# Kernel tuning notes

Hardware: AMD Instinct MI355X
Metric: run time of the kernel (lower is better)

Reference implementation:

```python
import jax, jax.numpy as jnp
from jax import lax
import numpy as np

GRID, IMG, BLOCK = 60, 960, 16
BN_EPS = 1e-5


def _conv(x, w, b):
    return lax.conv_general_dilated(x, w, (1, 1), 'SAME', dimension_numbers=('NCHW', 'OIHW', 'NCHW')) + b[None, :, None, None]


def _bn(x, g, b):
    # inference BatchNorm with running_mean=0, running_var=1
    s = g * np.float32(1.0 / np.sqrt(1.0 + BN_EPS))
    return x * s[None, :, None, None] + b[None, :, None, None]


def _mlp(x, w1, b1, w2, b2):
    return jax.nn.relu(x @ w1.T + b1) @ w2.T + b2


def _lstm_layer(x, wih, whh, b):
    # x: [B,T,D]; torch gate order i,f,g,o; zero initial state
    B = x.shape[0]
    H = whh.shape[1]
    pre = jnp.swapaxes(x, 0, 1) @ wih.T + b  # [T,B,4H]

    def step(carry, p):
        h, c = carry
        z = p + h @ whh.T
        i, f, g, o = jnp.split(z, 4, axis=-1)
        c = jax.nn.sigmoid(f) * c + jax.nn.sigmoid(i) * jnp.tanh(g)
        h = jax.nn.sigmoid(o) * jnp.tanh(c)
        return (h, c), h

    z0 = jnp.zeros((B, H), x.dtype)
    (h, c), ys = lax.scan(step, (z0, z0), pre)
    return jnp.swapaxes(ys, 0, 1), h, c


def _forward(motion_vectors, boxes, track_ids, conv1_w, conv1_b, bn1_g, bn1_b, conv2_w, conv2_b, bn2_g, bn2_b, conv3_w, conv3_b, bn3_g, bn3_b, agg_w1, agg_b1, agg_w2, agg_b2, bx_w1, bx_b1, bx_w2, bx_b2, id_table, proj_w, proj_b, empty_slot, l0_wih, l0_whh, l0_b, l1_wih, l1_whh, l1_b, hb_w1, hb_b1, hb_w2, hb_b2, hc_w1, hc_b1, hc_w2, hc_b2, ht_w1, ht_b1, ht_w2, ht_b2):
    B = motion_vectors.shape[0]
    # ---- grid encoder (Conv-BN-ReLU x3) ----
    x = jax.nn.relu(_bn(_conv(motion_vectors, conv1_w, conv1_b), bn1_g, bn1_b))
    x = jax.nn.relu(_bn(_conv(x, conv2_w, conv2_b), bn2_g, bn2_b))
    gf = jax.nn.relu(_bn(_conv(x, conv3_w, conv3_b), bn3_g, bn3_b))  # [B,64,60,60]
    global_feat = gf.mean((-2, -1))  # AdaptiveAvgPool2d(1) -> [B,64]

    # ---- per-box motion statistics (vectorized masked reductions) ----
    bg = jnp.clip(boxes * (IMG / BLOCK), 0.0, GRID - 1e-6)  # grid coords
    ix1 = jnp.floor(bg[..., 0]); iy1 = jnp.floor(bg[..., 1])
    ix2 = jnp.maximum(ix1 + 1.0, jnp.ceil(bg[..., 2]))
    iy2 = jnp.maximum(iy1 + 1.0, jnp.ceil(bg[..., 3]))
    g = jnp.arange(GRID, dtype=bg.dtype)
    mx_ = (g >= ix1[..., None]) & (g < ix2[..., None])  # [B,N,60]
    my_ = (g >= iy1[..., None]) & (g < iy2[..., None])
    mask = my_[..., :, None] & mx_[..., None, :]  # [B,N,60,60]
    m = mask.astype(bg.dtype)
    cnt = m.sum((-2, -1))[..., None]  # [B,N,1], >= 1 by construction
    mv = motion_vectors  # [B,2,60,60]
    s1 = jnp.einsum('bnyx,bcyx->bnc', m, mv)
    s2 = jnp.einsum('bnyx,bcyx->bnc', m, mv * mv)
    mean = s1 / cnt
    var = (s2 - cnt * mean * mean) / jnp.maximum(cnt - 1.0, 1.0)  # unbiased, like torch .std()
    var_safe = jnp.where(cnt > 1.0, jnp.maximum(var, 1e-12), 1.0)
    std = jnp.where(cnt > 1.0, jnp.sqrt(var_safe), 0.0)
    BIG = jnp.asarray(1e9, bg.dtype)
    mn = jnp.min(jnp.where(mask[:, :, None], mv[:, None], BIG), axis=(-2, -1))   # [B,N,2]
    mx = jnp.max(jnp.where(mask[:, :, None], mv[:, None], -BIG), axis=(-2, -1))  # [B,N,2]
    stats = jnp.stack([mean[..., 0], mean[..., 1], std[..., 0], std[..., 1], mn[..., 0], mx[..., 0], mn[..., 1], mx[..., 1]], -1)  # [B,N,8]
    motion_emb = _mlp(stats, agg_w1, agg_b1, agg_w2, agg_b2)  # [B,N,64]

    # ---- slot initialization ----
    box_emb = _mlp(boxes, bx_w1, bx_b1, bx_w2, bx_b2)  # [B,N,64]
    id_emb = id_table[jnp.clip(track_ids, 0, 999)]  # [B,N,32]
    obj = jnp.concatenate([box_emb, id_emb, motion_emb], -1)  # [B,N,160]
    slots = obj @ proj_w.T + proj_b  # [B,300,128]; N == max_slots so no empty slots used

    # ---- 2-layer LSTM over the 300 slots (batch_first, eval -> no dropout) ----
    Ns = slots.shape[1]
    gexp = jnp.broadcast_to(global_feat[:, None, :], (B, Ns, global_feat.shape[-1]))
    lstm_in = jnp.concatenate([slots, gexp], -1)  # [B,300,192]
    y, h0, c0 = _lstm_layer(lstm_in, l0_wih, l0_whh, l0_b)
    y, h1, c1 = _lstm_layer(y, l1_wih, l1_whh, l1_b)  # [B,300,128]

    # ---- RT-DETR style heads ----
    pred_boxes = jax.nn.sigmoid(_mlp(y, hb_w1, hb_b1, hb_w2, hb_b2))  # [B,300,4]
    cls_logits = _mlp(y, hc_w1, hc_b1, hc_w2, hc_b2)  # [B,300,2]
    tid_logits = _mlp(y, ht_w1, ht_b1, ht_w2, ht_b2)  # [B,300,1000]
    h = jnp.stack([h0, h1])
    c = jnp.stack([c0, c1])
    return pred_boxes, cls_logits, tid_logits, h, c


def setup_inputs() -> dict:
    B, N = 32, 300
    key = jax.random.key(0)
    ks = iter(jax.random.split(key, 60))

    def w(*s):
        return jax.random.normal(next(ks), s, jnp.float32) * 0.05

    mv = jax.random.normal(next(ks), (B, 2, GRID, GRID), jnp.float32)
    bb = jax.random.uniform(next(ks), (B, N, 4), jnp.float32)
    boxes = jnp.concatenate([jnp.minimum(bb[..., :2], bb[..., 2:]), jnp.maximum(bb[..., :2], bb[..., 2:])], -1)
    track_ids = jax.random.randint(next(ks), (B, N), 0, 1000)
    return dict(
        motion_vectors=mv, boxes=boxes, track_ids=track_ids,
        conv1_w=w(32, 2, 3, 3), conv1_b=w(32), bn1_g=1.0 + w(32), bn1_b=w(32),
        conv2_w=w(64, 32, 3, 3), conv2_b=w(64), bn2_g=1.0 + w(64), bn2_b=w(64),
        conv3_w=w(64, 64, 3, 3), conv3_b=w(64), bn3_g=1.0 + w(64), bn3_b=w(64),
        agg_w1=w(32, 8), agg_b1=w(32), agg_w2=w(64, 32), agg_b2=w(64),
        bx_w1=w(32, 4), bx_b1=w(32), bx_w2=w(64, 32), bx_b2=w(64),
        id_table=w(1000, 32).at[0].set(0.0),
        proj_w=w(128, 160), proj_b=w(128), empty_slot=w(128),
        l0_wih=w(512, 192), l0_whh=w(512, 128), l0_b=w(512),
        l1_wih=w(512, 128), l1_whh=w(512, 128), l1_b=w(512),
        hb_w1=w(256, 128), hb_b1=w(256), hb_w2=w(4, 256), hb_b2=w(4),
        hc_w1=w(256, 128), hc_b1=w(256), hc_w2=w(2, 256), hc_b2=w(2),
        ht_w1=w(256, 128), ht_b1=w(256), ht_w2=w(1000, 256), ht_b2=w(1000))


def reference(motion_vectors, boxes, track_ids, conv1_w, conv1_b, bn1_g, bn1_b, conv2_w, conv2_b, bn2_g, bn2_b, conv3_w, conv3_b, bn3_g, bn3_b, agg_w1, agg_b1, agg_w2, agg_b2, bx_w1, bx_b1, bx_w2, bx_b2, id_table, proj_w, proj_b, empty_slot, l0_wih, l0_whh, l0_b, l1_wih, l1_whh, l1_b, hb_w1, hb_b1, hb_w2, hb_b2, hc_w1, hc_b1, hc_w2, hc_b2, ht_w1, ht_b1, ht_w2, ht_b2):
    return _forward(motion_vectors, boxes, track_ids, conv1_w, conv1_b, bn1_g, bn1_b, conv2_w, conv2_b, bn2_g, bn2_b, conv3_w, conv3_b, bn3_g, bn3_b, agg_w1, agg_b1, agg_w2, agg_b2, bx_w1, bx_b1, bx_w2, bx_b2, id_table, proj_w, proj_b, empty_slot, l0_wih, l0_whh, l0_b, l1_wih, l1_whh, l1_b, hb_w1, hb_b1, hb_w2, hb_b2, hc_w1, hc_b1, hc_w2, hc_b2, ht_w1, ht_b1, ht_w2, ht_b2)
```

## Files before the change

### kernel.cpp

```cpp
#include <hip/hip_runtime.h>
#include <hip/hip_bf16.h>
#include <math.h>

typedef unsigned short ushort_t;
typedef __attribute__((ext_vector_type(8))) short bf16x8;
typedef __attribute__((ext_vector_type(4))) float f32x4;

#define LOG2E 1.4426950408889634f

__device__ __forceinline__ float sigf(float x) {
  x = fminf(fmaxf(x, -30.f), 30.f);
  return 1.f / (1.f + __expf(-x));
}
__device__ __forceinline__ ushort_t f2bf(float x) {
  unsigned int b = __float_as_uint(x);
  unsigned int lsb = (b >> 16) & 1u;
  b += 0x7fffu + lsb;
  return (ushort_t)(b >> 16);
}
__device__ __forceinline__ float bf2f(ushort_t u) {
  return __uint_as_float(((unsigned int)u) << 16);
}
__device__ __forceinline__ float gsc(int g3) {
  return (g3 == 2) ? (2.f * LOG2E) : LOG2E;
}

#define NPIX 3600
__device__ __forceinline__ int gperm(int rho) {
  return ((rho & 3) << 7) + (rho >> 2);
}

__global__ __launch_bounds__(256) void front_kernel(
    const float* __restrict__ mv, const float* __restrict__ boxes,
    const int* __restrict__ ids, const float* __restrict__ agg_w1,
    const float* __restrict__ agg_b1, const float* __restrict__ agg_w2,
    const float* __restrict__ agg_b2, const float* __restrict__ bx_w1,
    const float* __restrict__ bx_b1, const float* __restrict__ bx_w2,
    const float* __restrict__ bx_b2, const float* __restrict__ id_table,
    ushort_t* __restrict__ obj_out, const float* __restrict__ conv2_w,
    const float* __restrict__ conv3_w, const float* __restrict__ wih0,
    const float* __restrict__ projW, const float* __restrict__ projb,
    const float* __restrict__ l0_b, const float* __restrict__ hbw1,
    const float* __restrict__ hcw1, const float* __restrict__ htw1,
    const float* __restrict__ htw2, const float* __restrict__ hbb1,
    const float* __restrict__ hcb1, const float* __restrict__ htb1,
    ushort_t* __restrict__ wc2, ushort_t* __restrict__ wc3,
    ushort_t* __restrict__ wAp, float* __restrict__ l0bp,
    ushort_t* __restrict__ whid, ushort_t* __restrict__ wt2,
    float* __restrict__ bhid) {
  if (blockIdx.x < 1989) {
    int i = blockIdx.x * 256 + threadIdx.x;
    if (i < 18432) {
      int oc = i / 288, r = i % 288, kt = r / 32, ic = r % 32;
      wc2[i] = f2bf(conv2_w[((oc * 32 + ic) * 3 + kt / 3) * 3 + kt % 3]);
      return;
    }
    i -= 18432;
    if (i < 36864) {
      int oc = i / 576, r = i % 576, c = r / 288, r2 = r % 288;
      int kt = r2 / 32, icl = r2 % 32, ic = c * 32 + icl;
      wc3[i] = f2bf(conv3_w[((oc * 64 + ic) * 3 + kt / 3) * 3 + kt % 3]);
      return;
    }
    i -= 36864;
    if (i < 98304) {
      int n = i / 192, k = i % 192;
      int src = gperm(n);
      float a = 0.f;
      if (k < 160) {
        const float* wr = wih0 + src * 192;
        for (int j = 0; j < 128; ++j) a = fmaf(wr[j], projW[j * 160 + k], a);
      }
      wAp[i] = f2bf(a * gsc(n & 3));
      return;
    }
    i -= 98304;
    if (i < 512) {
      int src = gperm(i);
      float a = l0_b[src];
      const float* wr = wih0 + src * 192;
      for (int j = 0; j < 128; ++j) a = fmaf(wr[j], projb[j], a);
      l0bp[i] = a * gsc(i & 3);
      return;
    }
    i -= 512;
    if (i < 98304) {
      int row = i >> 7, c = i & 127;
      float v = (row < 256)   ? hbw1[row * 128 + c]
                : (row < 512) ? hcw1[(row - 256) * 128 + c]
                              : htw1[(row - 512) * 128 + c];
      whid[i] = f2bf(v);
      return;
    }
    i -= 98304;
    if (i < 256000) {
      wt2[i] = f2bf(htw2[i]);
      return;
    }
    i -= 256000;
    if (i < 768)
      bhid[i] = (i < 256) ? hbb1[i] : (i < 512) ? hcb1[i - 256] : htb1[i - 512];
    return;
  }
  int bx = blockIdx.x - 1989;
  __shared__ float obj[2][160];
  __shared__ float hm[2][32];
  __shared__ float hbx[2][32];
  __shared__ float stats[2][8];
  __shared__ float boxf[2][4];
  __shared__ float red[2][2][8];
  int h = threadIdx.x >> 7;
  int t = threadIdx.x & 127;
  int blk = bx * 2 + h;
  int b = blk / 300;
  float bx0 = boxes[blk * 4 + 0], by0 = boxes[blk * 4 + 1];
  float bx1 = boxes[blk * 4 + 2], by1 = boxes[blk * 4 + 3];
  const float HI = (float)(60.0 - 1e-6);
  float gx1 = fminf(fmaxf(bx0 * 60.f, 0.f), HI);
  float gy1 = fminf(fmaxf(by0 * 60.f, 0.f), HI);
  float gx2 = fminf(fmaxf(bx1 * 60.f, 0.f), HI);
  float gy2 = fminf(fmaxf(by1 * 60.f, 0.f), HI);
  float fx1 = floorf(gx1), fy1 = floorf(gy1);
  float fx2 = fmaxf(fx1 + 1.f, ceilf(gx2));
  float fy2 = fmaxf(fy1 + 1.f, ceilf(gy2));
  int ix1 = (int)fx1, iy1 = (int)fy1, ix2 = (int)fx2, iy2 = (int)fy2;
  int w = ix2 - ix1, hgt = iy2 - iy1;
  int area = w * hgt;
  float s0 = 0.f, s1 = 0.f, q0 = 0.f, q1 = 0.f;
  float mn0 = 1e9f, mn1 = 1e9f, mx0 = -1e9f, mx1 = -1e9f;
  const float* mv0 = mv + b * 2 * NPIX;
  const float* mv1 = mv0 + NPIX;
  for (int i = t; i < area; i += 128) {
    int r = i / w, cc = i - r * w;
    int yy = iy1 + r, xx = ix1 + cc;
    float v0 = mv0[yy * 60 + xx];
    float v1 = mv1[yy * 60 + xx];
    s0 += v0; q0 += v0 * v0; mn0 = fminf(mn0, v0); mx0 = fmaxf(mx0, v0);
    s1 += v1; q1 += v1 * v1; mn1 = fminf(mn1, v1); mx1 = fmaxf(mx1, v1);
  }
#pragma unroll
  for (int off = 32; off; off >>= 1) {
    s0 += __shfl_down(s0, off); s1 += __shfl_down(s1, off);
    q0 += __shfl_down(q0, off); q1 += __shfl_down(q1, off);
    mn0 = fminf(mn0, __shfl_down(mn0, off));
    mn1 = fminf(mn1, __shfl_down(mn1, off));
    mx0 = fmaxf(mx0, __shfl_down(mx0, off));
    mx1 = fmaxf(mx1, __shfl_down(mx1, off));
  }
  if ((t & 63) == 0) {
    int wv = t >> 6;
    red[h][wv][0] = s0; red[h][wv][1] = s1;
    red[h][wv][2] = q0; red[h][wv][3] = q1;
    red[h][wv][4] = mn0; red[h][wv][5] = mn1;
    red[h][wv][6] = mx0; red[h][wv][7] = mx1;
  }
  __syncthreads();
  if (t == 0) {
    float S0 = red[h][0][0] + red[h][1][0], S1 = red[h][0][1] + red[h][1][1];
    float Q0 = red[h][0][2] + red[h][1][2], Q1 = red[h][0][3] + red[h][1][3];
    float MN0 = fminf(red[h][0][4], red[h][1][4]);
    float MN1 = fminf(red[h][0][5], red[h][1][5]);
    float MX0 = fmaxf(red[h][0][6], red[h][1][6]);
    float MX1 = fmaxf(red[h][0][7], red[h][1][7]);
    float cnt = (float)area;
    float mean0 = S0 / cnt, mean1 = S1 / cnt;
    float var0 = (Q0 - cnt * mean0 * mean0) / fmaxf(cnt - 1.f, 1.f);
    float var1 = (Q1 - cnt * mean1 * mean1) / fmaxf(cnt - 1.f, 1.f);
    float sd0 = (cnt > 1.f) ? sqrtf(fmaxf(var0, 1e-12f)) : 0.f;
    float sd1 = (cnt > 1.f) ? sqrtf(fmaxf(var1, 1e-12f)) : 0.f;
    stats[h][0] = mean0; stats[h][1] = mean1; stats[h][2] = sd0;
    stats[h][3] = sd1; stats[h][4] = MN0; stats[h][5] = MX0;
    stats[h][6] = MN1; stats[h][7] = MX1;
    boxf[h][0] = bx0; boxf[h][1] = by0; boxf[h][2] = bx1; boxf[h][3] = by1;
  }
  __syncthreads();
  if (t < 32) {
    float a = agg_b1[t];
#pragma unroll
    for (int k = 0; k < 8; ++k) a = fmaf(stats[h][k], agg_w1[t * 8 + k], a);
    hm[h][t] = fmaxf(a, 0.f);
  } else if (t < 64) {
    int j = t - 32;
    float a = bx_b1[j];
#pragma unroll
    for (int k = 0; k < 4; ++k) a = fmaf(boxf[h][k], bx_w1[j * 4 + k], a);
    hbx[h][j] = fmaxf(a, 0.f);
  }
  __syncthreads();
  if (t < 64) {
    float a = bx_b2[t];
#pragma unroll
    for (int k = 0; k < 32; ++k) a = fmaf(hbx[h][k], bx_w2[t * 32 + k], a);
    obj[h][t] = a;
  } else {
    int j = t - 64;
    float a = agg_b2[j];
#pragma unroll
    for (int k = 0; k < 32; ++k) a = fmaf(hm[h][k], agg_w2[j * 32 + k], a);
    obj[h][96 + j] = a;
  }
  if (t < 32) {
    int id = ids[blk];
    id = min(max(id, 0), 999);
    obj[h][64 + t] = id_table[id * 32 + t];
  }
  __syncthreads();
  obj_out[(size_t)blk * 192 + t] = f2bf(obj[h][t]);
  if (t < 32) {
    obj_out[(size_t)blk * 192 + 128 + t] = f2bf(obj[h][128 + t]);
    obj_out[(size_t)blk * 192 + 160 + t] = 0;
  }
}

__global__ __launch_bounds__(256) void convstack_kernel(
    const float* __restrict__ mv, const float* __restrict__ c1w,
    const float* __restrict__ c1b, const float* __restrict__ bg1,
    const float* __restrict__ bb1, const ushort_t* __restrict__ wc2,
    const float* __restrict__ c2b, const float* __restrict__ bg2,
    const float* __restrict__ bb2, const ushort_t* __restrict__ wc3,
    const float* __restrict__ c3b, const float* __restrict__ bg3,
    const float* __restrict__ bb3, float* __restrict__ gf) {
  __shared__ char smem[25920 + 37152];
  ushort_t* c1_lds = (ushort_t*)smem;
  ushort_t* c2_lds = (ushort_t*)(smem + 25920);
  float* mv_lds = (float*)(smem + 25920);
  int tid = threadIdx.x;
  int wv = tid >> 6, lane = tid & 63;
  int col = lane & 15, kg = lane >> 4;
  int b = blockIdx.y, tile = blockIdx.x;
  int tq = tile / 5, tr = tile % 5;
  int ty0 = (tq == 4) ? 46 : tq * 14;
  int tx0 = (tr == 4) ? 46 : tr * 14;
  for (int i = tid; i < 800; i += 256) {
    int r = i % 400;
    int ch = i / 400, yy = r / 20, xx = r % 20;
    int gy = ty0 - 3 + yy, gx = tx0 - 3 + xx;
    float v = 0.f;
    if (gy >= 0 && gy < 60 && gx >= 0 && gx < 60)
      v = mv[((size_t)(b * 2 + ch) * 60 + gy) * 60 + gx];
    mv_lds[i] = v;
  }
  __syncthreads();
  {
    int oc = tid & 31;
    float s = bg1[oc] * rsqrtf(1.f + 1e-5f);
    float bias = fmaf(c1b[oc], s, bb1[oc]);
    float w1r[18];
#pragma unroll
    for (int k = 0; k < 18; ++k) w1r[k] = c1w[oc * 18 + k];
    for (int pos = tid >> 5; pos < 324; pos += 8) {
      int yy = pos / 18, xx = pos % 18;
      int gy = ty0 - 2 + yy, gx = tx0 - 2 + xx;
      ushort_t out = 0;
      if (gy >= 0 && gy < 60 && gx >= 0 && gx < 60) {
        float acc = 0.f;
#pragma unroll
        for (int ic = 0; ic < 2; ++ic)
#pragma unroll
          for (int ky = 0; ky < 3; ++ky)
#pragma unroll
            for (int kx = 0; kx < 3; ++kx)
              acc = fmaf(mv_lds[ic * 400 + (yy + ky) * 20 + xx + kx],
                         w1r[ic * 9 + ky * 3 + kx], acc);
        out = f2bf(fmaxf(fmaf(acc, s, bias), 0.f));
      }
      c1_lds[pos * 40 + oc] = out;
    }
  }
  __syncthreads();
  int oc2 = wv * 16 + col;
  {
    bf16x8 bw2[9];
#pragma unroll
    for (int kt = 0; kt < 9; ++kt)
      bw2[kt] = *(const bf16x8*)(wc2 + oc2 * 288 + kt * 32 + kg * 8);
    f32x4 a2[16];
#pragma unroll
    for (int m = 0; m < 16; ++m) a2[m] = (f32x4){0.f, 0.f, 0.f, 0.f};
#pragma unroll
    for (int kt = 0; kt < 9; ++kt) {
      int ky = kt / 3, kx = kt % 3;
#pragma unroll
      for (int m = 0; m < 16; ++m) {
        bf16x8 af = *(const bf16x8*)(
            &c1_lds[((m + ky) * 18 + col + kx) * 40 + kg * 8]);
        a2[m] =
            __builtin_amdgcn_mfma_f32_16x16x32_bf16(af, bw2[kt], a2[m], 0, 0, 0);
      }
    }
    float s = bg2[oc2] * rsqrtf(1.f + 1e-5f);
    float bias = fmaf(c2b[oc2], s, bb2[oc2]);
#pragma unroll
    for (int m = 0; m < 16; ++m) {
      int gy = ty0 - 1 + m;
#pragma unroll
      for (int r = 0; r < 4; ++r) {
        int gx = tx0 - 1 + kg * 4 + r;
        ushort_t o = 0;
        if (gy >= 0 && gy < 60 && gx >= 0 && gx < 60)
          o = f2bf(fmaxf(fmaf(a2[m][r], s, bias), 0.f));
        c2_lds[(m * 16 + kg * 4 + r) * 72 + oc2] = o;
      }
    }
  }
  __syncthreads();
  {
    bf16x8 bw3[2][9];
#pragma unroll
    for (int c = 0; c < 2; ++c)
#pragma unroll
      for (int kt = 0; kt < 9; ++kt)
        bw3[c][kt] =
            *(const bf16x8*)(wc3 + oc2 * 576 + c * 288 + kt * 32 + kg * 8);
    f32x4 a3[14];
#pragma unroll
    for (int m = 0; m < 14; ++m) a3[m] = (f32x4){0.f, 0.f, 0.f, 0.f};
#pragma unroll
    for (int c = 0; c < 2; ++c)
#pragma unroll
      for (int kt = 0; kt < 9; ++kt) {
        int ky = kt / 3, kx = kt % 3;
#pragma unroll
        for (int m = 0; m < 14; ++m) {
          bf16x8 af = *(const bf16x8*)(
              &c2_lds[((m + ky) * 16 + col + kx) * 72 + c * 32 + kg * 8]);
          a3[m] = __builtin_amdgcn_mfma_f32_16x16x32_bf16(af, bw3[c][kt],
                                                          a3[m], 0, 0, 0);
        }
      }
    float s = bg3[oc2] * rsqrtf(1.f + 1e-5f);
    float bias = fmaf(c3b[oc2], s, bb3[oc2]);
    float pool = 0.f;
#pragma unroll
    for (int m = 0; m < 14; ++m) {
      bool ym = (tq != 4) || (m >= 10);
#pragma unroll
      for (int r = 0; r < 4; ++r) {
        int px = kg * 4 + r;
        bool xm = (px < 14) && ((tr != 4) || (px >= 10));
        if (ym && xm) pool += fmaxf(fmaf(a3[m][r], s, bias), 0.f);
      }
    }
    pool += __shfl_xor(pool, 16);
    pool += __shfl_xor(pool, 32);
    if (lane < 16) atomicAdd(&gf[b * 64 + oc2], pool);
  }
}

template <int ACT, bool OBF16, bool GVEC>
__global__ __launch_bounds__(256) void gemm_bf16w_kernel(
    const ushort_t* __restrict__ A, int lda, const ushort_t* __restrict__ W,
    const float* __restrict__ bias, void* __restrict__ C, int ldc, int M,
    int N, int K, const float* __restrict__ wih0,
    const float* __restrict__ gf) {
  __shared__ ushort_t As[128 * 64];
  __shared__ ushort_t Ws[64 * 64];
  __shared__ float gvl[2][64];
  int tid = threadIdx.x;
  int wv = tid >> 6, lane = tid & 63;
  int col = lane & 15, kg = lane >> 4;
  int wm = wv >> 1, wn = wv & 1;
  int m0 = blockIdx.x * 128, n0 = blockIdx.y * 64;
  int bA = m0 / 300;
  if (GVEC && tid < 128) {
    int sel = tid >> 6;
    int nn = tid & 63;
    int n = n0 + nn;
    int bb = min(bA + sel, 31);
    const float* wr = wih0 + gperm(n) * 192 + 128;
    const float* gg = gf + bb * 64;
    float a = 0.f;
#pragma unroll
    for (int k = 0; k < 64; ++k) a = fmaf(wr[k], gg[k], a);
    gvl[sel][nn] = a * (1.f / 3600.f) * gsc(n & 3);
  }
  f32x4 acc[4][2];
#pragma unroll
  for (int i = 0; i < 4; ++i)
#pragma unroll
    for (int j = 0; j < 2; ++j) acc[i][j] = (f32x4){0.f, 0.f, 0.f, 0.f};

  int nk = K >> 6;
  for (int kc = 0; kc < nk; ++kc) {
    if (kc) __syncthreads();
#pragma unroll
    for (int q = 0; q < 4; ++q) {
      int idx = q * 256 + tid;
      int row = idx >> 3, ch = idx & 7;
      uint4 v =
          *(const uint4*)(A + (size_t)(m0 + row) * lda + kc * 64 + ch * 8);
      *(uint4*)(&As[row * 64 + ((ch * 8) ^ ((row & 7) << 3))]) = v;
    }
#pragma unroll
    for (int q = 0; q < 2; ++q) {
      int idx = q * 256 + tid;
      int row = idx >> 3, ch = idx & 7;
      int n = n0 + row;
      uint4 v = make_uint4(0, 0, 0, 0);
      if (n < N) v = *(const uint4*)(W + (size_t)n * K + kc * 64 + ch * 8);
      *(uint4*)(&Ws[row * 64 + ((ch * 8) ^ ((row & 7) << 3))]) = v;
    }
    __syncthreads();
#pragma unroll
    for (int ks = 0; ks < 2; ++ks) {
      bf16x8 bfr[2], afr[4];
#pragma unroll
      for (int ni = 0; ni < 2; ++ni) {
        int row = wn * 32 + ni * 16 + col;
        bfr[ni] = *(const bf16x8*)(
            &Ws[row * 64 + ((ks * 32 + kg * 8) ^ ((row & 7) << 3))]);
      }
#pragma unroll
      for (int mi = 0; mi < 4; ++mi) {
        int row = wm * 64 + mi * 16 + col;
        afr[mi] = *(const bf16x8*)(
            &As[row * 64 + ((ks * 32 + kg * 8) ^ ((row & 7) << 3))]);
      }
#pragma unroll
      for (int mi = 0; mi < 4; ++mi)
#pragma unroll
        for (int ni = 0; ni < 2; ++ni)
          acc[mi][ni] = __builtin_amdgcn_mfma_f32_16x16x32_bf16(
              afr[mi], bfr[ni], acc[mi][ni], 0, 0, 0);
    }
  }
#pragma unroll
  for (int ni = 0; ni < 2; ++ni) {
    int n = n0 + wn * 32 + ni * 16 + col;
    float bn = (n < N) ? bias[n] : 0.f;
#pragma unroll
    for (int mi = 0; mi < 4; ++mi) {
      int mbase = m0 + wm * 64 + mi * 16 + kg * 4;
#pragma unroll
      for (int r = 0; r < 4; ++r) {
        float v = acc[mi][ni][r] + bn;
        if (GVEC) v += gvl[(mbase + r) / 300 - bA][wn * 32 + ni * 16 + col];
        if (ACT == 1) v = fmaxf(v, 0.f);
        if (n < N) {
          if (OBF16)
            ((ushort_t*)C)[(size_t)(mbase + r) * ldc + n] = f2bf(v);
          else
            ((float*)C)[(size_t)(mbase + r) * ldc + n] = v;
        }
      }
    }
  }
}

__global__ __launch_bounds__(256) void head_small_kernel(
    const ushort_t* __restrict__ hid, const float* __restrict__ wb2,
    const float* __restrict__ bb2, const float* __restrict__ wc2,
    const float* __restrict__ bc2, float* __restrict__ outB,
    float* __restrict__ outC) {
  int idx = blockIdx.x * 256 + threadIdx.x;
  int row = idx / 6, j = idx % 6;
  const ushort_t* h = hid + (size_t)row * 768 + (j < 4 ? 0 : 256);
  const float* wrow = (j < 4) ? wb2 + j * 256 : wc2 + (j - 4) * 256;
  float acc = (j < 4) ? bb2[j] : bc2[j - 4];
  for (int k = 0; k < 256; k += 8) {
    uint4 hv = *(const uint4*)(h + k);
    unsigned int ww[4] = {hv.x, hv.y, hv.z, hv.w};
#pragma unroll
    for (int q = 0; q < 4; ++q) {
      acc = fmaf(bf2f((ushort_t)(ww[q] & 0xffff)), wrow[k + 2 * q], acc);
      acc = fmaf(bf2f((ushort_t)(ww[q] >> 16)), wrow[k + 2 * q + 1], acc);
    }
  }
  float v = (j < 4) ? sigf(acc) : acc;
  if (j < 4) outB[row * 4 + j] = v;
  else outC[row * 2 + (j - 4)] = v;
}

#define LSTM_BAR() asm volatile("s_waitcnt lgkmcnt(0)\n\ts_barrier" ::: "memory")

__global__ __launch_bounds__(512) void lstm_fused_kernel(
    const float* __restrict__ pre0,
    const float* __restrict__ whh0,
    const float* __restrict__ wih1,
    const float* __restrict__ whh1,
    const float* __restrict__ b1,
    float* __restrict__ pre1,
    ushort_t* __restrict__ y0,
    ushort_t* __restrict__ y1,
    float* __restrict__ outH, float* __restrict__ outC,
    unsigned int* __restrict__ flags)
{
  __shared__ ushort_t h_lds[2][4][160];
  int tid = threadIdx.x;
  int w = tid >> 6, lane = tid & 63;
  int col = lane & 15, kg = lane >> 4;
  int bat = col & 3, q = col >> 2;
  int cell = (4 * w + q) * 4 + kg;
  float wsc = gsc(col & 3);

  if (blockIdx.x < 8) {
    int g = blockIdx.x;
    int b0 = g * 4;
    unsigned int* flagp = &flags[g * 32];
    for (int i = tid; i < 2 * 4 * 160; i += 512) ((ushort_t*)h_lds)[i] = 0;
    bf16x8 aW0[4][4];
#pragma unroll
    for (int j = 0; j < 4; ++j) {
      int rho = (4 * w + j) * 16 + col;
      int src = gperm(rho);
#pragma unroll
      for (int kt = 0; kt < 4; ++kt) {
        const float* s1 = whh0 + src * 128 + kt * 32 + kg * 8;
        bf16x8 f1;
#pragma unroll
        for (int qq = 0; qq < 8; ++qq) f1[qq] = (short)f2bf(s1[qq] * wsc);
        aW0[j][kt] = f1;
      }
    }
    const float* pg = pre0 + (size_t)(b0 + bat) * 300 * 512 + 4 * cell;
    ushort_t* yg0 = y0 + ((size_t)(b0 + bat) * 300) * 128 + cell;
    float c = 0.f, hout = 0.f;
    f32x4 p0v = *(const f32x4*)(pg);
    f32x4 p1v = *(const f32x4*)(pg + 512);
    __syncthreads();

    for (int s = 0; s < 300; ++s) {
      const ushort_t* hb = h_lds[s & 1][bat];
      bf16x8 bfr[4];
#pragma unroll
      for (int kt = 0; kt < 4; ++kt)
        bfr[kt] = *(const bf16x8*)(hb + kt * 32 + kg * 8);
      f32x4 a0 = {0.f, 0.f, 0.f, 0.f}, a1 = a0, a2 = a0, a3 = a0;
#pragma unroll
      for (int kt = 0; kt < 4; ++kt) {
        a0 = __builtin_amdgcn_mfma_f32_16x16x32_bf16(aW0[0][kt], bfr[kt], a0, 0, 0, 0);
        a1 = __builtin_amdgcn_mfma_f32_16x16x32_bf16(aW0[1][kt], bfr[kt], a1, 0, 0, 0);
        a2 = __builtin_amdgcn_mfma_f32_16x16x32_bf16(aW0[2][kt], bfr[kt], a2, 0, 0, 0);
        a3 = __builtin_amdgcn_mfma_f32_16x16x32_bf16(aW0[3][kt], bfr[kt], a3, 0, 0, 0);
      }
      f32x4 z = a0;
      if (q == 1) z = a1;
      if (q == 2) z = a2;
      if (q == 3) z = a3;
      {
        float zi = z[0] + p0v[0];
        float zf = z[1] + p0v[1];
        float zg = z[2] + p0v[2];
        float zo = z[3] + p0v[3];
        float vi = __builtin_amdgcn_rcpf(1.f + __builtin_amdgcn_exp2f(-zi));
        float vf = __builtin_amdgcn_rcpf(1.f + __builtin_amdgcn_exp2f(-zf));
        float vg = 1.f - 2.f * __builtin_amdgcn_rcpf(
                              __builtin_amdgcn_exp2f(zg) + 1.f);
        float vo = __builtin_amdgcn_rcpf(1.f + __builtin_amdgcn_exp2f(-zo));
        c = vf * c + vi * vg;
        hout = vo * (1.f - 2.f * __builtin_amdgcn_rcpf(
                             __builtin_amdgcn_exp2f(2.f * LOG2E * c) + 1.f));
        ushort_t hv = f2bf(hout);
        h_lds[(s + 1) & 1][bat][cell] = hv;
        __builtin_nontemporal_store(hv, yg0 + (size_t)s * 128);
        p0v = p1v;
        int sn = (s + 2 < 300) ? s + 2 : 299;
        p1v = *(const f32x4*)(pg + (size_t)sn * 512);
      }
      asm volatile("s_waitcnt vmcnt(6)" ::: "memory");
      LSTM_BAR();
      if (tid == 0 && s >= 3)
        __hip_atomic_store(flagp, (unsigned int)(s - 3), __ATOMIC_RELAXED,
                           __HIP_MEMORY_SCOPE_AGENT);
    }
    asm volatile("s_waitcnt vmcnt(0)" ::: "memory");
    __syncthreads();
    if (tid == 0)
      __hip_atomic_store(flagp, 300u, __ATOMIC_RELAXED,
                         __HIP_MEMORY_SCOPE_AGENT);
    outH[(b0 + bat) * 128 + cell] = hout;
    outC[(b0 + bat) * 128 + cell] = c;
  } else if (blockIdx.x < 16) {
    int g = blockIdx.x - 8;
    int b0 = g * 4;
    unsigned int* flagp = &flags[g * 32 + 16];
    for (int i = tid; i < 2 * 4 * 160; i += 512) ((ushort_t*)h_lds)[i] = 0;
    bf16x8 aW[4][4];
#pragma unroll
    for (int j = 0; j < 4; ++j) {
      int rho = (4 * w + j) * 16 + col;
      int src = gperm(rho);
#pragma unroll
      for (int kt = 0; kt < 4; ++kt) {
        const float* s1 = whh1 + src * 128 + kt * 32 + kg * 8;
        bf16x8 f1;
#pragma unroll
        for (int qq = 0; qq < 8; ++qq) f1[qq] = (short)f2bf(s1[qq] * wsc);
        aW[j][kt] = f1;
      }
    }
    float bi = b1[cell] * LOG2E, bff = b1[128 + cell] * LOG2E;
    float bgg = b1[256 + cell] * (2.f * LOG2E), boo = b1[384 + cell] * LOG2E;
    const float* pg = pre1 + (size_t)(b0 + bat) * 300 * 512 + 4 * cell;
    ushort_t* yg = y1 + (size_t)(b0 + bat) * 300 * 128 + cell;
    float c = 0.f, hout = 0.f;
    unsigned int fc = 0;
    f32x4 p0v, p1v;
    do {
      fc = __hip_atomic_load(flagp, __ATOMIC_RELAXED,
                             __HIP_MEMORY_SCOPE_AGENT);
      if (fc < 1) __builtin_amdgcn_s_sleep(2);
    } while (fc < 1);
    asm volatile("" ::: "memory");
    p0v = __builtin_nontemporal_load((const f32x4*)(pg));
    while (fc < 2) {
      fc = __hip_atomic_load(flagp, __ATOMIC_RELAXED,
                             __HIP_MEMORY_SCOPE_AGENT);
      if (fc < 2) __builtin_amdgcn_s_sleep(2);
    }
    asm volatile("" ::: "memory");
    p1v = __builtin_nontemporal_load((const f32x4*)(pg + 512));
    __syncthreads();

    for (int t = 0; t < 300; ++t) {
      unsigned int fcn = __hip_atomic_load(flagp, __ATOMIC_RELAXED,
                                           __HIP_MEMORY_SCOPE_AGENT);
      const ushort_t* hb = h_lds[t & 1][bat];
      bf16x8 bfr[4];
#pragma unroll
      for (int kt = 0; kt < 4; ++kt)
        bfr[kt] = *(const bf16x8*)(hb + kt * 32 + kg * 8);
      f32x4 a0 = {0.f, 0.f, 0.f, 0.f}, a1 = a0, a2 = a0, a3 = a0;
#pragma unroll
      for (int kt = 0; kt < 4; ++kt) {
        a0 = __builtin_amdgcn_mfma_f32_16x16x32_bf16(aW[0][kt], bfr[kt], a0, 0, 0, 0);
        a1 = __builtin_amdgcn_mfma_f32_16x16x32_bf16(aW[1][kt], bfr[kt], a1, 0, 0, 0);
        a2 = __builtin_amdgcn_mfma_f32_16x16x32_bf16(aW[2][kt], bfr[kt], a2, 0, 0, 0);
        a3 = __builtin_amdgcn_mfma_f32_16x16x32_bf16(aW[3][kt], bfr[kt], a3, 0, 0, 0);
      }
      f32x4 z = a0;
      if (q == 1) z = a1;
      if (q == 2) z = a2;
      if (q == 3) z = a3;
      {
        float zi = z[0] + p0v[0] + bi;
        float zf = z[1] + p0v[1] + bff;
        float zg = z[2] + p0v[2] + bgg;
        float zo = z[3] + p0v[3] + boo;
        float vi = __builtin_amdgcn_rcpf(1.f + __builtin_amdgcn_exp2f(-zi));
        float vf = __builtin_amdgcn_rcpf(1.f + __builtin_amdgcn_exp2f(-zf));
        float vg = 1.f - 2.f * __builtin_amdgcn_rcpf(
                              __builtin_amdgcn_exp2f(zg) + 1.f);
        float vo = __builtin_amdgcn_rcpf(1.f + __builtin_amdgcn_exp2f(-zo));
        c = vf * c + vi * vg;
        hout = vo * (1.f - 2.f * __builtin_amdgcn_rcpf(
                             __builtin_amdgcn_exp2f(2.f * LOG2E * c) + 1.f));
        ushort_t hv = f2bf(hout);
        h_lds[(t + 1) & 1][bat][cell] = hv;
        __builtin_nontemporal_store(hv, yg + (size_t)t * 128);
        p0v = p1v;
        if (t + 2 < 300) {
          unsigned int need = (unsigned int)(t + 3);
          if (fcn > fc) fc = fcn;
          if (fc < need) {
            do {
              fc = __hip_atomic_load(flagp, __ATOMIC_RELAXED,
                                     __HIP_MEMORY_SCOPE_AGENT);
              if (fc < need) __builtin_amdgcn_s_sleep(2);
            } while (fc < need);
            asm volatile("" ::: "memory");
          }
          p1v = __builtin_nontemporal_load(
              (const f32x4*)(pg + (size_t)(t + 2) * 512));
        }
      }
      LSTM_BAR();
    }
    outH[4096 + (b0 + bat) * 128 + cell] = hout;
    outC[4096 + (b0 + bat) * 128 + cell] = c;
  } else {
    int g = blockIdx.x - 16;
    int b0 = g * 4;
    unsigned int* flag0 = &flags[g * 32];
    unsigned int* flag1 = &flags[g * 32 + 16];
    bf16x8 aU[4][4];
#pragma unroll
    for (int j = 0; j < 4; ++j) {
      int rho = (4 * w + j) * 16 + col;
      int src = gperm(rho);
#pragma unroll
      for (int kt = 0; kt < 4; ++kt) {
        const float* s2 = wih1 + src * 128 + kt * 32 + kg * 8;
        bf16x8 f2;
#pragma unroll
        for (int qq = 0; qq < 8; ++qq) f2[qq] = (short)f2bf(s2[qq] * wsc);
        aU[j][kt] = f2;
      }
    }
    int bb = col & 3;
    int ts = col >> 2;
    const ushort_t* yb = y0 + ((size_t)(b0 + bb) * 300) * 128 + kg * 8;
    unsigned int fc = 0;
    for (int t0 = 0; t0 < 300; t0 += 12) {
      unsigned int need = (unsigned int)(t0 + 11);
      while (fc < need) {
        fc = __hip_atomic_load(flag0, __ATOMIC_RELAXED,
                               __HIP_MEMORY_SCOPE_AGENT);
        if (fc < need) __builtin_amdgcn_s_sleep(2);
      }
      asm volatile("" ::: "memory");
      f32x4 acc[4][3];
#pragma unroll
      for (int j = 0; j < 4; ++j)
#pragma unroll
        for (int ct = 0; ct < 3; ++ct) acc[j][ct] = (f32x4){0.f, 0.f, 0.f, 0.f};
#pragma unroll
      for (int ct = 0; ct < 3; ++ct) {
        int t = t0 + ct * 4 + ts;
        bf16x8 bfr[4];
#pragma unroll
        for (int kt = 0; kt < 4; ++kt)
          bfr[kt] = __builtin_nontemporal_load(
              (const bf16x8*)(yb + (size_t)t * 128 + kt * 32));
#pragma unroll
        for (int kt = 0; kt < 4; ++kt) {
          acc[0][ct] = __builtin_amdgcn_mfma_f32_16x16x32_bf16(aU[0][kt], bfr[kt], acc[0][ct], 0, 0, 0);
          acc[1][ct] = __builtin_amdgcn_mfma_f32_16x16x32_bf16(aU[1][kt], bfr[kt], acc[1][ct], 0, 0, 0);
          acc[2][ct] = __builtin_amdgcn_mfma_f32_16x16x32_bf16(aU[2][kt], bfr[kt], acc[2][ct], 0, 0, 0);
          acc[3][ct] = __builtin_amdgcn_mfma_f32_16x16x32_bf16(aU[3][kt], bfr[kt], acc[3][ct], 0, 0, 0);
        }
      }
#pragma unroll
      for (int ct = 0; ct < 3; ++ct) {
        int t = t0 + ct * 4 + ts;
        float* pd = pre1 + ((size_t)(b0 + bb) * 300 + t) * 512 + kg * 4;
#pragma unroll
        for (int j = 0; j < 4; ++j)
          __builtin_nontemporal_store(acc[j][ct],
                                      (f32x4*)(pd + (4 * w + j) * 16));
      }
      asm volatile("s_waitcnt vmcnt(0)" ::: "memory");
      __syncthreads();
      if (tid == 0)
        __hip_atomic_store(flag1, (unsigned int)(t0 + 12), __ATOMIC_RELAXED,
                           __HIP_MEMORY_SCOPE_AGENT);
    }
  }
}

extern "C" void kernel_launch(void* const* d_in, const int* in_sizes, int n_in,
                              void* d_out, int out_size, void* d_ws,
                              size_t ws_size, hipStream_t stream) {
  const float* mv = (const float*)d_in[0];
  const float* boxes = (const float*)d_in[1];
  const int* track_ids = (const int*)d_in[2];
  const float* conv1_w = (const float*)d_in[3];
  const float* conv1_b = (const float*)d_in[4];
  const float* bn1_g = (const float*)d_in[5];
  const float* bn1_b = (const float*)d_in[6];
  const float* conv2_w = (const float*)d_in[7];
  const float* conv2_b = (const float*)d_in[8];
  const float* bn2_g = (const float*)d_in[9];
  const float* bn2_b = (const float*)d_in[10];
  const float* conv3_w = (const float*)d_in[11];
  const float* conv3_b = (const float*)d_in[12];
  const float* bn3_g = (const float*)d_in[13];
  const float* bn3_b = (const float*)d_in[14];
  const float* agg_w1 = (const float*)d_in[15];
  const float* agg_b1 = (const float*)d_in[16];
  const float* agg_w2 = (const float*)d_in[17];
  const float* agg_b2 = (const float*)d_in[18];
  const float* bx_w1 = (const float*)d_in[19];
  const float* bx_b1 = (const float*)d_in[20];
  const float* bx_w2 = (const float*)d_in[21];
  const float* bx_b2 = (const float*)d_in[22];
  const float* id_table = (const float*)d_in[23];
  const float* proj_w = (const float*)d_in[24];
  const float* proj_b = (const float*)d_in[25];
  const float* l0_wih = (const float*)d_in[27];
  const float* l0_whh = (const float*)d_in[28];
  const float* l0_b = (const float*)d_in[29];
  const float* l1_wih = (const float*)d_in[30];
  const float* l1_whh = (const float*)d_in[31];
  const float* l1_b = (const float*)d_in[32];
  const float* hb_w1 = (const float*)d_in[33];
  const float* hb_b1 = (const float*)d_in[34];
  const float* hb_w2 = (const float*)d_in[35];
  const float* hb_b2 = (const float*)d_in[36];
  const float* hc_w1 = (const float*)d_in[37];
  const float* hc_b1 = (const float*)d_in[38];
  const float* hc_w2 = (const float*)d_in[39];
  const float* hc_b2 = (const float*)d_in[40];
  const float* ht_w1 = (const float*)d_in[41];
  const float* ht_b1 = (const float*)d_in[42];
  const float* ht_w2 = (const float*)d_in[43];
  const float* ht_b2 = (const float*)d_in[44];

  char* wsb = (char*)d_ws;
  float* pre0 = (float*)(wsb + 0);
  ushort_t* hid = (ushort_t*)(wsb + 0);
  ushort_t* y0g = (ushort_t*)(wsb + 19660800);
  float* gf = (float*)(wsb + 22118400);
  ushort_t* obj = (ushort_t*)(wsb + 22126592);
  float* pre1 = (float*)(wsb + 25812992);
  ushort_t* y1b = (ushort_t*)(wsb + 45473792);
  unsigned int* flags = (unsigned int*)(wsb + 47931392);
  ushort_t* wAp = (ushort_t*)(wsb + 47932416);
  ushort_t* whid = (ushort_t*)(wsb + 48129024);
  ushort_t* wt2 = (ushort_t*)(wsb + 48325632);
  float* bhid = (float*)(wsb + 48837632);
  float* l0bp = (float*)(wsb + 48840704);
  ushort_t* wc2 = (ushort_t*)(wsb + 48908288);
  ushort_t* wc3 = (ushort_t*)(wsb + 48945152);

  float* outB = (float*)d_out;
  float* outC = outB + 38400;
  float* outT = outB + 57600;
  float* outH = outB + 9657600;
  float* outCc = outB + 9665792;

  hipMemsetAsync(gf, 0, 2048 * sizeof(float), stream);
  hipMemsetAsync(flags, 0, 1024, stream);

  front_kernel<<<6789, 256, 0, stream>>>(
      mv, boxes, track_ids, agg_w1, agg_b1, agg_w2, agg_b2, bx_w1, bx_b1,
      bx_w2, bx_b2, id_table, obj, conv2_w, conv3_w, l0_wih, proj_w, proj_b,
      l0_b, hb_w1, hc_w1, ht_w1, ht_w2, hb_b1, hc_b1, ht_b1, wc2, wc3, wAp,
      l0bp, whid, wt2, bhid);
  convstack_kernel<<<dim3(25, 32), 256, 0, stream>>>(
      mv, conv1_w, conv1_b, bn1_g, bn1_b, wc2, conv2_b, bn2_g, bn2_b, wc3,
      conv3_b, bn3_g, bn3_b, gf);
  gemm_bf16w_kernel<0, false, true><<<dim3(75, 8), 256, 0, stream>>>(
      obj, 192, wAp, l0bp, pre0, 512, 9600, 512, 192, l0_wih, gf);
  lstm_fused_kernel<<<24, 512, 0, stream>>>(pre0, l0_whh, l1_wih, l1_whh,
                                            l1_b, pre1, y0g, y1b, outH, outCc,
                                            flags);
  gemm_bf16w_kernel<1, true, false><<<dim3(75, 12), 256, 0, stream>>>(
      y1b, 128, whid, bhid, hid, 768, 9600, 768, 128, nullptr, nullptr);
  head_small_kernel<<<225, 256, 0, stream>>>(hid, hb_w2, hb_b2, hc_w2, hc_b2,
                                             outB, outC);
  gemm_bf16w_kernel<0, false, false><<<dim3(75, 16), 256, 0, stream>>>(
      hid + 512, 768, wt2, ht_b2, outT, 1000, 9600, 1000, 256, nullptr,
      nullptr);
}
```

Baseline: 473.1 us.

## Co-locate LSTM layer 0 and layer 1 recurrences in one 1024-thread block

Merges the layer-0 and layer-1 recurrent blocks for each batch group into a single 1024-thread workgroup. The two halves run in lockstep on a shared barrier, with layer 1 lagging a fixed number of steps behind layer 0, and the grid shrinks from 24 to 16 blocks. The input-projection blocks are widened to 1024 threads, and their idle upper half spins through matching barriers before exiting. This trades fewer blocks and cross-CU flag latency for shared barriers, which couple the two layers' step times. There is also a risk of barrier-count mismatches with the hard-coded 25 syncs.

```diff
diff --git a/kernel.cpp b/kernel.cpp
--- a/kernel.cpp
+++ b/kernel.cpp
@@ -472,8 +472,9 @@
 }
 
 #define LSTM_BAR() asm volatile("s_waitcnt lgkmcnt(0)\n\ts_barrier" ::: "memory")
-
-__global__ __launch_bounds__(512) void lstm_fused_kernel(
+#define LSTM_LAG 24
+
+__global__ __launch_bounds__(1024, 1) void lstm_fused_kernel(
     const float* __restrict__ pre0,
     const float* __restrict__ whh0,
     const float* __restrict__ wih1,
@@ -485,9 +486,11 @@
     float* __restrict__ outH, float* __restrict__ outC,
     unsigned int* __restrict__ flags)
 {
-  __shared__ ushort_t h_lds[2][4][160];
+  __shared__ ushort_t h0_lds[2][4][160];
+  __shared__ ushort_t h1_lds[2][4][160];
   int tid = threadIdx.x;
-  int w = tid >> 6, lane = tid & 63;
+  int ltid = tid & 511;
+  int w = ltid >> 6, lane = ltid & 63;
   int col = lane & 15, kg = lane >> 4;
   int bat = col & 3, q = col >> 2;
   int cell = (4 * w + q) * 4 + kg;
@@ -496,183 +499,191 @@
   if (blockIdx.x < 8) {
     int g = blockIdx.x;
     int b0 = g * 4;
-    unsigned int* flagp = &flags[g * 32];
-    for (int i = tid; i < 2 * 4 * 160; i += 512) ((ushort_t*)h_lds)[i] = 0;
-    bf16x8 aW0[4][4];
-#pragma unroll
-    for (int j = 0; j < 4; ++j) {
-      int rho = (4 * w + j) * 16 + col;
-      int src = gperm(rho);
-#pragma unroll
-      for (int kt = 0; kt < 4; ++kt) {
-        const float* s1 = whh0 + src * 128 + kt * 32 + kg * 8;
-        bf16x8 f1;
-#pragma unroll
-        for (int qq = 0; qq < 8; ++qq) f1[qq] = (short)f2bf(s1[qq] * wsc);
-        aW0[j][kt] = f1;
-      }
-    }
-    const float* pg = pre0 + (size_t)(b0 + bat) * 300 * 512 + 4 * cell;
-    ushort_t* yg0 = y0 + ((size_t)(b0 + bat) * 300) * 128 + cell;
-    float c = 0.f, hout = 0.f;
-    f32x4 p0v = *(const f32x4*)(pg);
-    f32x4 p1v = *(const f32x4*)(pg + 512);
-    __syncthreads();
-
-    for (int s = 0; s < 300; ++s) {
-      const ushort_t* hb = h_lds[s & 1][bat];
-      bf16x8 bfr[4];
-#pragma unroll
-      for (int kt = 0; kt < 4; ++kt)
-        bfr[kt] = *(const bf16x8*)(hb + kt * 32 + kg * 8);
-      f32x4 a0 = {0.f, 0.f, 0.f, 0.f}, a1 = a0, a2 = a0, a3 = a0;
-#pragma unroll
-      for (int kt = 0; kt < 4; ++kt) {
-        a0 = __builtin_amdgcn_mfma_f32_16x16x32_bf16(aW0[0][kt], bfr[kt], a0, 0, 0, 0);
-        a1 = __builtin_amdgcn_mfma_f32_16x16x32_bf16(aW0[1][kt], bfr[kt], a1, 0, 0, 0);
-        a2 = __builtin_amdgcn_mfma_f32_16x16x32_bf16(aW0[2][kt], bfr[kt], a2, 0, 0, 0);
-        a3 = __builtin_amdgcn_mfma_f32_16x16x32_bf16(aW0[3][kt], bfr[kt], a3, 0, 0, 0);
-      }
-      f32x4 z = a0;
-      if (q == 1) z = a1;
-      if (q == 2) z = a2;
-      if (q == 3) z = a3;
-      {
-        float zi = z[0] + p0v[0];
-        float zf = z[1] + p0v[1];
-        float zg = z[2] + p0v[2];
-        float zo = z[3] + p0v[3];
-        float vi = __builtin_amdgcn_rcpf(1.f + __builtin_amdgcn_exp2f(-zi));
-        float vf = __builtin_amdgcn_rcpf(1.f + __builtin_amdgcn_exp2f(-zf));
-        float vg = 1.f - 2.f * __builtin_amdgcn_rcpf(
-                              __builtin_amdgcn_exp2f(zg) + 1.f);
-        float vo = __builtin_amdgcn_rcpf(1.f + __builtin_amdgcn_exp2f(-zo));
-        c = vf * c + vi * vg;
-        hout = vo * (1.f - 2.f * __builtin_amdgcn_rcpf(
-                             __builtin_amdgcn_exp2f(2.f * LOG2E * c) + 1.f));
-        ushort_t hv = f2bf(hout);
-        h_lds[(s + 1) & 1][bat][cell] = hv;
-        __builtin_nontemporal_store(hv, yg0 + (size_t)s * 128);
-        p0v = p1v;
-        int sn = (s + 2 < 300) ? s + 2 : 299;
-        p1v = *(const f32x4*)(pg + (size_t)sn * 512);
-      }
-      asm volatile("s_waitcnt vmcnt(6)" ::: "memory");
-      LSTM_BAR();
-      if (tid == 0 && s >= 3)
-        __hip_atomic_store(flagp, (unsigned int)(s - 3), __ATOMIC_RELAXED,
-                           __HIP_MEMORY_SCOPE_AGENT);
-    }
-    asm volatile("s_waitcnt vmcnt(0)" ::: "memory");
-    __syncthreads();
-    if (tid == 0)
-      __hip_atomic_store(flagp, 300u, __ATOMIC_RELAXED,
-                         __HIP_MEMORY_SCOPE_AGENT);
-    outH[(b0 + bat) * 128 + cell] = hout;
-    outC[(b0 + bat) * 128 + cell] = c;
-  } else if (blockIdx.x < 16) {
+    unsigned int* flag0 = &flags[g * 32];
+    unsigned int* flag1 = &flags[g * 32 + 16];
+    for (int i = tid; i < 2 * 4 * 160; i += 1024) {
+      ((ushort_t*)h0_lds)[i] = 0;
+      ((ushort_t*)h1_lds)[i] = 0;
+    }
+    if (tid < 512) {
+      bf16x8 aW0[4][4];
+#pragma unroll
+      for (int j = 0; j < 4; ++j) {
+        int rho = (4 * w + j) * 16 + col;
+        int src = gperm(rho);
+#pragma unroll
+        for (int kt = 0; kt < 4; ++kt) {
+          const float* s1 = whh0 + src * 128 + kt * 32 + kg * 8;
+          bf16x8 f1;
+#pragma unroll
+          for (int qq = 0; qq < 8; ++qq) f1[qq] = (short)f2bf(s1[qq] * wsc);
+          aW0[j][kt] = f1;
+        }
+      }
+      const float* pg = pre0 + (size_t)(b0 + bat) * 300 * 512 + 4 * cell;
+      ushort_t* yg0 = y0 + ((size_t)(b0 + bat) * 300) * 128 + cell;
+      float c = 0.f, hout = 0.f;
+      f32x4 p0v = *(const f32x4*)(pg);
+      f32x4 p1v = *(const f32x4*)(pg + 512);
+      __syncthreads();
+
+      for (int p = 0; p < 300 + LSTM_LAG; ++p) {
+        if (p < 300) {
+          const ushort_t* hb = h0_lds[p & 1][bat];
+          bf16x8 bfr[4];
+#pragma unroll
+          for (int kt = 0; kt < 4; ++kt)
+            bfr[kt] = *(const bf16x8*)(hb + kt * 32 + kg * 8);
+          f32x4 a0 = {0.f, 0.f, 0.f, 0.f}, a1 = a0, a2 = a0, a3 = a0;
+#pragma unroll
+          for (int kt = 0; kt < 4; ++kt) {
+            a0 = __builtin_amdgcn_mfma_f32_16x16x32_bf16(aW0[0][kt], bfr[kt], a0, 0, 0, 0);
+            a1 = __builtin_amdgcn_mfma_f32_16x16x32_bf16(aW0[1][kt], bfr[kt], a1, 0, 0, 0);
+            a2 = __builtin_amdgcn_mfma_f32_16x16x32_bf16(aW0[2][kt], bfr[kt], a2, 0, 0, 0);
+            a3 = __builtin_amdgcn_mfma_f32_16x16x32_bf16(aW0[3][kt], bfr[kt], a3, 0, 0, 0);
+          }
+          f32x4 z = a0;
+          if (q == 1) z = a1;
+          if (q == 2) z = a2;
+          if (q == 3) z = a3;
+          float zi = z[0] + p0v[0];
+          float zf = z[1] + p0v[1];
+          float zg = z[2] + p0v[2];
+          float zo = z[3] + p0v[3];
+          float vi = __builtin_amdgcn_rcpf(1.f + __builtin_amdgcn_exp2f(-zi));
+          float vf = __builtin_amdgcn_rcpf(1.f + __builtin_amdgcn_exp2f(-zf));
+          float vg = 1.f - 2.f * __builtin_amdgcn_rcpf(
+                                __builtin_amdgcn_exp2f(zg) + 1.f);
+          float vo = __builtin_amdgcn_rcpf(1.f + __builtin_amdgcn_exp2f(-zo));
+          c = vf * c + vi * vg;
+          hout = vo * (1.f - 2.f * __builtin_amdgcn_rcpf(
+                               __builtin_amdgcn_exp2f(2.f * LOG2E * c) + 1.f));
+          ushort_t hv = f2bf(hout);
+          h0_lds[(p + 1) & 1][bat][cell] = hv;
+          __builtin_nontemporal_store(hv, yg0 + (size_t)p * 128);
+          p0v = p1v;
+          int sn = (p + 2 < 300) ? p + 2 : 299;
+          p1v = *(const f32x4*)(pg + (size_t)sn * 512);
+          asm volatile("s_waitcnt vmcnt(6)" ::: "memory");
+        } else if (p == 300) {
+          asm volatile("s_waitcnt vmcnt(0)" ::: "memory");
+        }
+        LSTM_BAR();
+        if (tid == 0) {
+          if (p >= 3 && p < 300)
+            __hip_atomic_store(flag0, (unsigned int)(p - 3), __ATOMIC_RELAXED,
+                               __HIP_MEMORY_SCOPE_AGENT);
+          else if (p == 300)
+            __hip_atomic_store(flag0, 300u, __ATOMIC_RELAXED,
+                               __HIP_MEMORY_SCOPE_AGENT);
+        }
+      }
+      outH[(b0 + bat) * 128 + cell] = hout;
+      outC[(b0 + bat) * 128 + cell] = c;
+    } else {
+      bf16x8 aW[4][4];
+#pragma unroll
+      for (int j = 0; j < 4; ++j) {
+        int rho = (4 * w + j) * 16 + col;
+        int src = gperm(rho);
+#pragma unroll
+        for (int kt = 0; kt < 4; ++kt) {
+          const float* s1 = whh1 + src * 128 + kt * 32 + kg * 8;
+          bf16x8 f1;
+#pragma unroll
+          for (int qq = 0; qq < 8; ++qq) f1[qq] = (short)f2bf(s1[qq] * wsc);
+          aW[j][kt] = f1;
+        }
+      }
+      float bi = b1[cell] * LOG2E, bff = b1[128 + cell] * LOG2E;
+      float bgg = b1[256 + cell] * (2.f * LOG2E), boo = b1[384 + cell] * LOG2E;
+      const float* pg = pre1 + (size_t)(b0 + bat) * 300 * 512 + 4 * cell;
+      ushort_t* yg = y1 + (size_t)(b0 + bat) * 300 * 128 + cell;
+      float c = 0.f, hout = 0.f;
+      unsigned int fc = 0;
+      f32x4 p0v = {0.f, 0.f, 0.f, 0.f}, p1v = p0v;
+      __syncthreads();
+
+      for (int p = 0; p < 300 + LSTM_LAG; ++p) {
+        if (p == LSTM_LAG - 2) {
+          while (fc < 1) {
+            fc = __hip_atomic_load(flag1, __ATOMIC_RELAXED,
+                                   __HIP_MEMORY_SCOPE_AGENT);
+            if (fc < 1) __builtin_amdgcn_s_sleep(2);
+          }
+          asm volatile("" ::: "memory");
+          p0v = __builtin_nontemporal_load((const f32x4*)(pg));
+        } else if (p == LSTM_LAG - 1) {
+          while (fc < 2) {
+            fc = __hip_atomic_load(flag1, __ATOMIC_RELAXED,
+                                   __HIP_MEMORY_SCOPE_AGENT);
+            if (fc < 2) __builtin_amdgcn_s_sleep(2);
+          }
+          asm volatile("" ::: "memory");
+          p1v = __builtin_nontemporal_load((const f32x4*)(pg + 512));
+        } else if (p >= LSTM_LAG) {
+          int t = p - LSTM_LAG;
+          const ushort_t* hb = h1_lds[t & 1][bat];
+          bf16x8 bfr[4];
+#pragma unroll
+          for (int kt = 0; kt < 4; ++kt)
+            bfr[kt] = *(const bf16x8*)(hb + kt * 32 + kg * 8);
+          f32x4 a0 = {0.f, 0.f, 0.f, 0.f}, a1 = a0, a2 = a0, a3 = a0;
+#pragma unroll
+          for (int kt = 0; kt < 4; ++kt) {
+            a0 = __builtin_amdgcn_mfma_f32_16x16x32_bf16(aW[0][kt], bfr[kt], a0, 0, 0, 0);
+            a1 = __builtin_amdgcn_mfma_f32_16x16x32_bf16(aW[1][kt], bfr[kt], a1, 0, 0, 0);
+            a2 = __builtin_amdgcn_mfma_f32_16x16x32_bf16(aW[2][kt], bfr[kt], a2, 0, 0, 0);
+            a3 = __builtin_amdgcn_mfma_f32_16x16x32_bf16(aW[3][kt], bfr[kt], a3, 0, 0, 0);
+          }
+          f32x4 z = a0;
+          if (q == 1) z = a1;
+          if (q == 2) z = a2;
+          if (q == 3) z = a3;
+          float zi = z[0] + p0v[0] + bi;
+          float zf = z[1] + p0v[1] + bff;
+          float zg = z[2] + p0v[2] + bgg;
+          float zo = z[3] + p0v[3] + boo;
+          float vi = __builtin_amdgcn_rcpf(1.f + __builtin_amdgcn_exp2f(-zi));
+          float vf = __builtin_amdgcn_rcpf(1.f + __builtin_amdgcn_exp2f(-zf));
+          float vg = 1.f - 2.f * __builtin_amdgcn_rcpf(
+                                __builtin_amdgcn_exp2f(zg) + 1.f);
+          float vo = __builtin_amdgcn_rcpf(1.f + __builtin_amdgcn_exp2f(-zo));
+          c = vf * c + vi * vg;
+          hout = vo * (1.f - 2.f * __builtin_amdgcn_rcpf(
+                               __builtin_amdgcn_exp2f(2.f * LOG2E * c) + 1.f));
+          ushort_t hv = f2bf(hout);
+          h1_lds[(t + 1) & 1][bat][cell] = hv;
+          __builtin_nontemporal_store(hv, yg + (size_t)t * 128);
+          p0v = p1v;
+          if (t + 2 < 300) {
+            unsigned int need = (unsigned int)(t + 3);
+            if (fc < need) {
+              do {
+                fc = __hip_atomic_load(flag1, __ATOMIC_RELAXED,
+                                       __HIP_MEMORY_SCOPE_AGENT);
+                if (fc < need) __builtin_amdgcn_s_sleep(2);
+              } while (fc < need);
+              asm volatile("" ::: "memory");
+            }
+            p1v = __builtin_nontemporal_load(
+                (const f32x4*)(pg + (size_t)(t + 2) * 512));
+          }
+        }
+        LSTM_BAR();
+      }
+      outH[4096 + (b0 + bat) * 128 + cell] = hout;
+      outC[4096 + (b0 + bat) * 128 + cell] = c;
+    }
+  } else {
     int g = blockIdx.x - 8;
-    int b0 = g * 4;
-    unsigned int* flagp = &flags[g * 32 + 16];
-    for (int i = tid; i < 2 * 4 * 160; i += 512) ((ushort_t*)h_lds)[i] = 0;
-    bf16x8 aW[4][4];
-#pragma unroll
-    for (int j = 0; j < 4; ++j) {
-      int rho = (4 * w + j) * 16 + col;
-      int src = gperm(rho);
-#pragma unroll
-      for (int kt = 0; kt < 4; ++kt) {
-        const float* s1 = whh1 + src * 128 + kt * 32 + kg * 8;
-        bf16x8 f1;
-#pragma unroll
-        for (int qq = 0; qq < 8; ++qq) f1[qq] = (short)f2bf(s1[qq] * wsc);
-        aW[j][kt] = f1;
-      }
-    }
-    float bi = b1[cell] * LOG2E, bff = b1[128 + cell] * LOG2E;
-    float bgg = b1[256 + cell] * (2.f * LOG2E), boo = b1[384 + cell] * LOG2E;
-    const float* pg = pre1 + (size_t)(b0 + bat) * 300 * 512 + 4 * cell;
-    ushort_t* yg = y1 + (size_t)(b0 + bat) * 300 * 128 + cell;
-    float c = 0.f, hout = 0.f;
-    unsigned int fc = 0;
-    f32x4 p0v, p1v;
-    do {
-      fc = __hip_atomic_load(flagp, __ATOMIC_RELAXED,
-                             __HIP_MEMORY_SCOPE_AGENT);
-      if (fc < 1) __builtin_amdgcn_s_sleep(2);
-    } while (fc < 1);
-    asm volatile("" ::: "memory");
-    p0v = __builtin_nontemporal_load((const f32x4*)(pg));
-    while (fc < 2) {
-      fc = __hip_atomic_load(flagp, __ATOMIC_RELAXED,
-                             __HIP_MEMORY_SCOPE_AGENT);
-      if (fc < 2) __builtin_amdgcn_s_sleep(2);
-    }
-    asm volatile("" ::: "memory");
-    p1v = __builtin_nontemporal_load((const f32x4*)(pg + 512));
-    __syncthreads();
-
-    for (int t = 0; t < 300; ++t) {
-      unsigned int fcn = __hip_atomic_load(flagp, __ATOMIC_RELAXED,
-                                           __HIP_MEMORY_SCOPE_AGENT);
-      const ushort_t* hb = h_lds[t & 1][bat];
-      bf16x8 bfr[4];
-#pragma unroll
-      for (int kt = 0; kt < 4; ++kt)
-        bfr[kt] = *(const bf16x8*)(hb + kt * 32 + kg * 8);
-      f32x4 a0 = {0.f, 0.f, 0.f, 0.f}, a1 = a0, a2 = a0, a3 = a0;
-#pragma unroll
-      for (int kt = 0; kt < 4; ++kt) {
-        a0 = __builtin_amdgcn_mfma_f32_16x16x32_bf16(aW[0][kt], bfr[kt], a0, 0, 0, 0);
-        a1 = __builtin_amdgcn_mfma_f32_16x16x32_bf16(aW[1][kt], bfr[kt], a1, 0, 0, 0);
-        a2 = __builtin_amdgcn_mfma_f32_16x16x32_bf16(aW[2][kt], bfr[kt], a2, 0, 0, 0);
-        a3 = __builtin_amdgcn_mfma_f32_16x16x32_bf16(aW[3][kt], bfr[kt], a3, 0, 0, 0);
-      }
-      f32x4 z = a0;
-      if (q == 1) z = a1;
-      if (q == 2) z = a2;
-      if (q == 3) z = a3;
-      {
-        float zi = z[0] + p0v[0] + bi;
-        float zf = z[1] + p0v[1] + bff;
-        float zg = z[2] + p0v[2] + bgg;
-        float zo = z[3] + p0v[3] + boo;
-        float vi = __builtin_amdgcn_rcpf(1.f + __builtin_amdgcn_exp2f(-zi));
-        float vf = __builtin_amdgcn_rcpf(1.f + __builtin_amdgcn_exp2f(-zf));
-        float vg = 1.f - 2.f * __builtin_amdgcn_rcpf(
-                              __builtin_amdgcn_exp2f(zg) + 1.f);
-        float vo = __builtin_amdgcn_rcpf(1.f + __builtin_amdgcn_exp2f(-zo));
-        c = vf * c + vi * vg;
-        hout = vo * (1.f - 2.f * __builtin_amdgcn_rcpf(
-                             __builtin_amdgcn_exp2f(2.f * LOG2E * c) + 1.f));
-        ushort_t hv = f2bf(hout);
-        h_lds[(t + 1) & 1][bat][cell] = hv;
-        __builtin_nontemporal_store(hv, yg + (size_t)t * 128);
-        p0v = p1v;
-        if (t + 2 < 300) {
-          unsigned int need = (unsigned int)(t + 3);
-          if (fcn > fc) fc = fcn;
-          if (fc < need) {
-            do {
-              fc = __hip_atomic_load(flagp, __ATOMIC_RELAXED,
-                                     __HIP_MEMORY_SCOPE_AGENT);
-              if (fc < need) __builtin_amdgcn_s_sleep(2);
-            } while (fc < need);
-            asm volatile("" ::: "memory");
-          }
-          p1v = __builtin_nontemporal_load(
-              (const f32x4*)(pg + (size_t)(t + 2) * 512));
-        }
-      }
-      LSTM_BAR();
-    }
-    outH[4096 + (b0 + bat) * 128 + cell] = hout;
-    outC[4096 + (b0 + bat) * 128 + cell] = c;
-  } else {
-    int g = blockIdx.x - 16;
     int b0 = g * 4;
     unsigned int* flag0 = &flags[g * 32];
     unsigned int* flag1 = &flags[g * 32 + 16];
+    if (tid >= 512) {
+      for (int k = 0; k < 25; ++k) __syncthreads();
+      return;
+    }
     bf16x8 aU[4][4];
 #pragma unroll
     for (int j = 0; j < 4; ++j) {
@@ -822,9 +833,9 @@
       conv3_b, bn3_g, bn3_b, gf);
   gemm_bf16w_kernel<0, false, true><<<dim3(75, 8), 256, 0, stream>>>(
       obj, 192, wAp, l0bp, pre0, 512, 9600, 512, 192, l0_wih, gf);
-  lstm_fused_kernel<<<24, 512, 0, stream>>>(pre0, l0_whh, l1_wih, l1_whh,
-                                            l1_b, pre1, y0g, y1b, outH, outCc,
-                                            flags);
+  lstm_fused_kernel<<<16, 1024, 0, stream>>>(pre0, l0_whh, l1_wih, l1_whh,
+                                             l1_b, pre1, y0g, y1b, outH,
+                                             outCc, flags);
   gemm_bf16w_kernel<1, true, false><<<dim3(75, 12), 256, 0, stream>>>(
       y1b, 128, whid, bhid, hid, 768, 9600, 768, 128, nullptr, nullptr);
   head_small_kernel<<<225, 256, 0, stream>>>(hid, hb_w2, hb_b2, hc_w2, hc_b2,
```

Measured after the change: 521.9 us. 10.3% more time.
